# Optimization experiments

Hardware: AMD Instinct MI355X
Metric: run time of the kernel (lower is better)

The kernel has to match this reference:

```python
import jax, jax.numpy as jnp
import numpy as np
from jax import lax

B, DIM, H, W = 2, 96, 256, 256
HEADS, WIN = 4, 8
HID = int(DIM * 2.66)  # ffn hidden_features = 255


def setup_inputs() -> dict:
    key = jax.random.key(0)
    ks = jax.random.split(key, 8)
    s = 0.02
    return {
        "x": jax.random.normal(ks[0], (B, DIM, H, W), jnp.float32),
        "to_hidden_w": jax.random.normal(ks[1], (6 * DIM, DIM), jnp.float32) * s,
        "to_hidden_dw_w": jax.random.normal(ks[2], (6 * DIM, 1, 3, 3), jnp.float32) * s,
        "project_out_w": jax.random.normal(ks[3], (DIM, 2 * DIM), jnp.float32) * s,
        "temperature": jnp.ones((HEADS, 1, 1, 1), jnp.float32),
        "norm1_w": jnp.ones((DIM,), jnp.float32),
        "norm2_w": jnp.ones((DIM,), jnp.float32),
        "ffn_in_w": jax.random.normal(ks[4], (2 * HID, DIM), jnp.float32) * s,
        "ffn_dw_w": jax.random.normal(ks[5], (2 * HID, 1, 3, 3), jnp.float32) * s,
        "ffn_out_w": jax.random.normal(ks[6], (DIM, HID), jnp.float32) * s,
    }


def _ln_biasfree(x, w):
    # BiasFree_LayerNorm over channel dim (torch var over last dim of b,(hw),c)
    v = jnp.var(x, axis=1, keepdims=True)
    return x / jnp.sqrt(v + 1e-5) * w[None, :, None, None]


def _conv1x1(x, w):
    return jnp.einsum('bchw,oc->bohw', x, w)


def _dwconv3(x, w):
    return lax.conv_general_dilated(x, w, (1, 1), [(1, 1), (1, 1)],
                                    feature_group_count=x.shape[1],
                                    dimension_numbers=('NCHW', 'OIHW', 'NCHW'))


def _to_patch(t):
    # b (head c) (h p1) (w p2) -> b head (h w) c (p1 p2)
    b, hc, hh, ww = t.shape
    c, h, w = hc // HEADS, hh // WIN, ww // WIN
    t = t.reshape(b, HEADS, c, h, WIN, w, WIN)
    t = t.transpose(0, 1, 3, 5, 2, 4, 6)
    return t.reshape(b, HEADS, h * w, c, WIN * WIN)


def _from_patch(t, hh, ww):
    # b head (h w) c (p1 p2) -> b (head c) (h p1) (w p2)
    b, hd, hw, c, pp = t.shape
    h, w = hh // WIN, ww // WIN
    t = t.reshape(b, hd, h, w, c, WIN, WIN)
    t = t.transpose(0, 1, 4, 2, 5, 3, 6)
    return t.reshape(b, hd * c, hh, ww)


def _attn(x, to_hidden_w, to_hidden_dw_w, project_out_w, temperature):
    hh, ww = x.shape[-2:]
    hidden = _dwconv3(_conv1x1(x, to_hidden_w), to_hidden_dw_w)
    q, k, v = jnp.split(hidden, 3, axis=1)
    qf = jnp.fft.rfft(_to_patch(q), axis=-1)
    kf = jnp.fft.rfft(_to_patch(k), axis=-1)
    vf = jnp.fft.rfft(_to_patch(v), axis=-1)
    attn = jnp.einsum('bhpcf,bhpcg->bhpfg', qf, kf) * temperature[None]
    nrm = jnp.sqrt(jnp.sum(jnp.abs(attn) ** 2, axis=-1, keepdims=True))  # complex last-dim vector norm
    attn = attn / nrm
    out = jnp.einsum('bhpfg,bhpcg->bhpcf', attn, vf)  # (attn @ vf^T)^T -> b head p c f
    out = jnp.fft.irfft(out, n=WIN * WIN, axis=-1)
    return _conv1x1(_from_patch(out, hh, ww), project_out_w)


def _ffn(x, w_in, w_dw, w_out):
    t = _dwconv3(_conv1x1(x, w_in), w_dw)
    x1, x2 = jnp.split(t, 2, axis=1)
    return _conv1x1(jax.nn.gelu(x1, approximate=False) * x2, w_out)


def reference(x, to_hidden_w, to_hidden_dw_w, project_out_w, temperature,
              norm1_w, norm2_w, ffn_in_w, ffn_dw_w, ffn_out_w):
    x = x + _attn(_ln_biasfree(x, norm1_w), to_hidden_w, to_hidden_dw_w,
                  project_out_w, temperature)
    x = x + _ffn(_ln_biasfree(x, norm2_w), ffn_in_w, ffn_dw_w, ffn_out_w)
    return x
```

## Files before the change

### kernel.cpp

```cpp
#include <hip/hip_runtime.h>
#include <hip/hip_bf16.h>
#include <math.h>

#define HW 65536
typedef __hip_bfloat16 bf16;
typedef __attribute__((ext_vector_type(8))) short short8;
typedef __attribute__((ext_vector_type(4))) float float4v;

__device__ __forceinline__ float bf2f(bf16 h) { return __bfloat162float(h); }
__device__ __forceinline__ bf16  f2bf(float f) { return __float2bfloat16(f); }
__device__ __forceinline__ float bflo(unsigned u){ return __uint_as_float(u << 16); }
__device__ __forceinline__ float bfhi(unsigned u){ return __uint_as_float(u & 0xffff0000u); }
__device__ __forceinline__ float bits2f(unsigned short u){ return __uint_as_float(((unsigned)u) << 16); }
__device__ __forceinline__ unsigned short f2bfbits(float f){
  bf16 h = __float2bfloat16(f);
  unsigned short u; __builtin_memcpy(&u, &h, 2); return u;
}
__device__ __forceinline__ bool io_is_f32(const unsigned short* tflag) {
  return tflag[0] == 0;
}
#define C64 0.09817477042468103f

__global__ __launch_bounds__(256) void convert_params(
    const void* p1, const void* p2, const void* p3, const void* p4,
    const void* p5, const void* p6, const void* p7, const void* p8,
    const void* p9, bf16* dst) {
  int i = blockIdx.x * 256 + threadIdx.x;
  if (i >= 157042) return;
  bool f32 = io_is_f32((const unsigned short*)p4);
  #define RD(src, j) (f32 ? ((const float*)(src))[j] : bits2f(((const unsigned short*)(src))[j]))
  float v;
  if      (i < 55296)  { v = RD(p1, i) * RD(p5, i % 96); }
  else if (i < 60480)  { v = RD(p2, i - 55296); }
  else if (i < 78912)  { v = RD(p3, i - 60480); }
  else if (i < 78916)  { v = RD(p4, i - 78912); }
  else if (i < 127876) { int j = i - 78916;  v = RD(p7, j) * RD(p6, j % 96); }
  else if (i < 132466) { v = RD(p8, i - 127876); }
  else {
    int j = i - 132466;
    int o = j >> 8, c = j & 255;
    v = (c < 255) ? RD(p9, o*255 + c) : 0.f;
  }
  #undef RD
  dst[i] = f2bf(v);
}

template<bool EXT>
__global__ __launch_bounds__(256) void ln_pre(const void* __restrict__ in,
                                              bf16* __restrict__ out, size_t eoff,
                                              const unsigned short* __restrict__ tflag) {
  int t = blockIdx.x * 256 + threadIdx.x;
  int p = t >> 1;
  int half = t & 1;
  const bool f32 = EXT && io_is_f32(tflag);
  float v[48];
  float s = 0.f, s2 = 0.f;
  #pragma unroll
  for (int j = 0; j < 48; ++j) {
    size_t off = (size_t)(half*48 + j) * HW + p;
    float xv = EXT ? (f32 ? ((const float*)in)[eoff + off]
                          : bits2f(((const unsigned short*)in)[eoff + off]))
                   : bits2f(((const unsigned short*)in)[off]);
    v[j] = xv; s += xv; s2 += xv*xv;
  }
  s  += __shfl_xor(s, 1);
  s2 += __shfl_xor(s2, 1);
  float mean = s * (1.f/96.f);
  float var  = s2 * (1.f/96.f) - mean*mean;
  float inv  = rsqrtf(fmaxf(var, 0.f) + 1e-5f);
  #pragma unroll
  for (int j = 0; j < 48; ++j)
    out[(size_t)(half*48 + j) * HW + p] = f2bf(v[j] * inv);
}

template<int CIN, int K32, int KP, int PT, int OT, int WAVES, bool RES,
         bool RESEXT, bool OUTEXT, bool PERM>
__global__ __launch_bounds__(WAVES*64) void conv_mfma(
    const bf16* __restrict__ in, const bf16* __restrict__ w,
    const void* __restrict__ res,
    void* __restrict__ out, size_t eoff,
    const unsigned short* __restrict__ tflag, int cout) {
  constexpr int BT = WAVES * 64;
  constexpr int NT = PT / 16;
  constexpr int MT = OT / (16 * WAVES);
  constexpr int SOS = PT + 8;
  __shared__ __align__(16) unsigned short SH[PT*KP + OT*KP];
  unsigned short (*in_lds)[KP] = (unsigned short(*)[KP])SH;
  unsigned short (*w_lds)[KP]  = (unsigned short(*)[KP])(SH + PT*KP);
  const int tid = threadIdx.x;
  const int p0 = blockIdx.x * PT;
  const int ob = blockIdx.y * OT;
  const bool iof32 = (RESEXT || OUTEXT) ? io_is_f32(tflag) : false;
  const unsigned short* inu = (const unsigned short*)in;
  const unsigned short* wu  = (const unsigned short*)w;

  #define ROTS(r) ({ int _s = (((r) >> 3) << 3); if (_s >= K32) _s -= K32; _s; })

  for (int i = tid; i < CIN*(PT/8); i += BT) {
    int c = i / (PT/8), p8 = (i % (PT/8)) * 8;
    uint4 v = *(const uint4*)&inu[(size_t)c*HW + p0 + p8];
    unsigned short e[8];
    e[0] = (unsigned short)(v.x); e[1] = (unsigned short)(v.x >> 16);
    e[2] = (unsigned short)(v.y); e[3] = (unsigned short)(v.y >> 16);
    e[4] = (unsigned short)(v.z); e[5] = (unsigned short)(v.z >> 16);
    e[6] = (unsigned short)(v.w); e[7] = (unsigned short)(v.w >> 16);
    #pragma unroll
    for (int j = 0; j < 8; ++j) {
      int row = p8 + j;
      int pc = c + ROTS(row);
      if (pc >= K32) pc -= K32;
      in_lds[row][pc] = e[j];
    }
  }
  for (int i = tid; i < OT*(K32/8); i += BT) {
    int ol = i / (K32/8), cb = (i % (K32/8)) * 8;
    int o = ob + ol;
    uint4 v = make_uint4(0u, 0u, 0u, 0u);
    if (o < cout) v = *(const uint4*)&wu[(size_t)o*K32 + cb];
    *(uint4*)&w_lds[ol][cb] = v;
  }
  if (K32 > CIN) {
    for (int i = tid; i < (K32 - CIN) * PT; i += BT) {
      int row = i % PT, lc = CIN + i / PT;
      int pc = lc + ROTS(row);
      if (pc >= K32) pc -= K32;
      in_lds[row][pc] = 0;
    }
  }
  __syncthreads();

  const int lane = tid & 63, wave = tid >> 6;
  const int col = lane & 15, quad = lane >> 4;
  float4v acc[MT][NT];
  #pragma unroll
  for (int mt = 0; mt < MT; ++mt)
    #pragma unroll
    for (int nt = 0; nt < NT; ++nt)
      acc[mt][nt] = (float4v){0.f, 0.f, 0.f, 0.f};

  #pragma unroll
  for (int ks = 0; ks < K32/32; ++ks) {
    const int kb = ks*32 + quad*8;
    short8 a[MT];
    #pragma unroll
    for (int mt = 0; mt < MT; ++mt)
      a[mt] = *(const short8*)&w_lds[(wave + WAVES*mt)*16 + col][kb];
    #pragma unroll
    for (int nt = 0; nt < NT; ++nt) {
      const int row = nt*16 + col;
      int pkb = kb + ROTS(row);
      if (pkb >= K32) pkb -= K32;
      short8 bfr = *(const short8*)&in_lds[row][pkb];
      #pragma unroll
      for (int mt = 0; mt < MT; ++mt)
        acc[mt][nt] = __builtin_amdgcn_mfma_f32_16x16x32_bf16(a[mt], bfr, acc[mt][nt], 0, 0, 0);
    }
  }
  #undef ROTS

  __syncthreads();
  unsigned short* Sout = SH;
  #pragma unroll
  for (int mt = 0; mt < MT; ++mt) {
    #pragma unroll
    for (int nt = 0; nt < NT; ++nt) {
      const int p = nt*16 + col;
      #pragma unroll
      for (int r = 0; r < 4; ++r) {
        int ol = (wave + WAVES*mt)*16 + quad*4 + r;
        Sout[ol*SOS + p] = f2bfbits(acc[mt][nt][r]);
      }
    }
  }
  __syncthreads();

  for (int j = tid; j < OT*(PT/8); j += BT) {
    int ol = j / (PT/8), seg = j % (PT/8);
    int o = ob + ol;
    if (o >= cout) continue;
    int p = seg*8;
    int nat;
    if (PERM) {
      int pg = p0 + p;
      int window = pg >> 6, e = pg & 63;
      nat = (((window >> 5)*8 + (e >> 3)) << 8) + ((window & 31) << 3);
    } else {
      nat = p0 + p;
    }
    size_t oi = (size_t)o * HW + nat;
    uint4 hv = *(const uint4*)&Sout[ol*SOS + p];
    if (!RES && !(OUTEXT)) {
      *(uint4*)((unsigned short*)out + oi) = hv;
      continue;
    }
    float f0=bflo(hv.x), f1=bfhi(hv.x), f2=bflo(hv.y), f3=bfhi(hv.y);
    float f4=bflo(hv.z), f5=bfhi(hv.z), f6=bflo(hv.w), f7=bfhi(hv.w);
    if (RES) {
      if (RESEXT && iof32) {
        const float* rp = (const float*)res + eoff + oi;
        float4 r0 = *(const float4*)rp;
        float4 r1 = *(const float4*)(rp + 4);
        f0+=r0.x; f1+=r0.y; f2+=r0.z; f3+=r0.w;
        f4+=r1.x; f5+=r1.y; f6+=r1.z; f7+=r1.w;
      } else {
        const unsigned short* rp = (const unsigned short*)res + (RESEXT ? eoff + oi : oi);
        uint4 rv = *(const uint4*)rp;
        f0+=bflo(rv.x); f1+=bfhi(rv.x); f2+=bflo(rv.y); f3+=bfhi(rv.y);
        f4+=bflo(rv.z); f5+=bfhi(rv.z); f6+=bflo(rv.w); f7+=bfhi(rv.w);
      }
    }
    if (OUTEXT && iof32) {
      float* op = (float*)out + eoff + oi;
      *(float4*)op       = make_float4(f0, f1, f2, f3);
      *(float4*)(op + 4) = make_float4(f4, f5, f6, f7);
    } else {
      uint4 ov;
      ov.x = f2bfbits(f0) | ((unsigned)f2bfbits(f1) << 16);
      ov.y = f2bfbits(f2) | ((unsigned)f2bfbits(f3) << 16);
      ov.z = f2bfbits(f4) | ((unsigned)f2bfbits(f5) << 16);
      ov.w = f2bfbits(f6) | ((unsigned)f2bfbits(f7) << 16);
      *(uint4*)((unsigned short*)out + (OUTEXT ? eoff + oi : oi)) = ov;
    }
  }
}

__device__ __forceinline__ void dw9x8(const unsigned short* __restrict__ pin,
                                      const bf16* __restrict__ w,
                                      int y, int x0, float* __restrict__ o) {
  float wv[9];
  #pragma unroll
  for (int i = 0; i < 9; ++i) wv[i] = bf2f(w[i]);
  float r[3][10];
  #pragma unroll
  for (int dy = 0; dy < 3; ++dy) {
    int yy = y + dy - 1;
    if (yy < 0 || yy > 255) {
      #pragma unroll
      for (int j = 0; j < 10; ++j) r[dy][j] = 0.f;
    } else {
      const unsigned short* row = pin + yy*256 + x0;
      uint4 q = *(const uint4*)row;
      r[dy][1] = bflo(q.x); r[dy][2] = bfhi(q.x);
      r[dy][3] = bflo(q.y); r[dy][4] = bfhi(q.y);
      r[dy][5] = bflo(q.z); r[dy][6] = bfhi(q.z);
      r[dy][7] = bflo(q.w); r[dy][8] = bfhi(q.w);
      r[dy][0] = (x0 > 0)   ? bits2f(row[-1]) : 0.f;
      r[dy][9] = (x0 < 248) ? bits2f(row[8])  : 0.f;
    }
  }
  #pragma unroll
  for (int j = 0; j < 8; ++j) {
    float s = 0.f;
    #pragma unroll
    for (int dy = 0; dy < 3; ++dy)
      #pragma unroll
      for (int dx = 0; dx < 3; ++dx)
        s += r[dy][j+dx] * wv[dy*3+dx];
    o[j] = s;
  }
}

__global__ __launch_bounds__(256) void dwconv_gate_v8(const bf16* __restrict__ in,
                                                      const bf16* __restrict__ w,
                                                      bf16* __restrict__ out) {
  int t = blockIdx.x * 256 + threadIdx.x;
  int g8 = t & 8191;
  int c  = t >> 13;
  int y  = g8 >> 5;
  int x0 = (g8 & 31) << 3;
  float d1[8], d2[8];
  dw9x8((const unsigned short*)in + ((size_t)c << 16),         w + c*9,       y, x0, d1);
  dw9x8((const unsigned short*)in + ((size_t)(c+255) << 16),   w + (c+255)*9, y, x0, d2);
  unsigned short ob[8];
  #pragma unroll
  for (int j = 0; j < 8; ++j) {
    float g = 0.5f * d1[j] * (1.f + erff(d1[j] * 0.70710678118654752f)) * d2[j];
    ob[j] = f2bfbits(g);
  }
  uint4 ov;
  ov.x = ob[0] | ((unsigned)ob[1] << 16);
  ov.y = ob[2] | ((unsigned)ob[3] << 16);
  ov.z = ob[4] | ((unsigned)ob[5] << 16);
  ov.w = ob[6] | ((unsigned)ob[7] << 16);
  *(uint4*)((unsigned short*)out + ((size_t)c << 16) + y*256 + x0) = ov;
}

__global__ __launch_bounds__(512, 8) void fft_attn_mfma(const bf16* __restrict__ hid,
                                                        const bf16* __restrict__ temp,
                                                        bf16* __restrict__ outP,
                                                        const bf16* __restrict__ wdw) {
  constexpr int RS  = 68;
  constexpr int MS  = 100;
  constexpr int RAW = 0;
  constexpr int WFo = 9792;
  constexpr int QAo = 0;
  constexpr int KB1 = 4800;
  constexpr int KB2 = 9600;
  constexpr int VAo = 14400;
  constexpr int AB1 = 0;
  constexpr int AB2 = 4800;
  constexpr int OAo = 9600;
  constexpr int WIo = 0;
  __shared__ __align__(16) unsigned short S[19200];
  __shared__ float inv_s[48];

  const int tid = threadIdx.x;
  const int lane = tid & 63, wave = tid >> 6;
  const int col = lane & 15, quad = lane >> 4;

  const int bid = blockIdx.x;
  const int sw  = ((bid & 7) << 9) | (bid >> 3);
  const int head = sw >> 10;
  const int patch = sw & 1023;
  const int y0 = (patch >> 5) * 8, x0 = (patch & 31) * 8;
  const float tscale = bf2f(temp[head]);
  const unsigned short* hidu = (const unsigned short*)hid;

  for (int i = tid; i < 1152; i += 512) {
    int tc = i >> 3, wr = i & 7;
    int chan = (tc/48)*192 + head*48 + (tc%48);
    float o[8];
    dw9x8(hidu + ((size_t)chan << 16), wdw + chan*9, y0 + wr, x0, o);
    unsigned short* d = &S[RAW + tc*RS + wr*8];
    uint2 lo = make_uint2(f2bfbits(o[0]) | ((unsigned)f2bfbits(o[1]) << 16),
                          f2bfbits(o[2]) | ((unsigned)f2bfbits(o[3]) << 16));
    uint2 hi = make_uint2(f2bfbits(o[4]) | ((unsigned)f2bfbits(o[5]) << 16),
                          f2bfbits(o[6]) | ((unsigned)f2bfbits(o[7]) << 16));
    *(uint2*)d       = lo;
    *(uint2*)(d + 4) = hi;
  }
  for (int i = tid; i < 80*64; i += 512) {
    int n = i >> 6, e = i & 63;
    float v = 0.f;
    if (n < 33)      v =  __builtin_amdgcn_cosf((float)((n*e) & 63) * 0.015625f);
    else if (n < 66) v = -__builtin_amdgcn_sinf((float)(((n-33)*e) & 63) * 0.015625f);
    S[WFo + n*RS + e] = f2bfbits(v);
  }
  __syncthreads();

  float4v dacc[6];
  #pragma unroll
  for (int k = 0; k < 6; ++k) {
    int ti = wave + 8*k;
    if (ti < 45) {
      int mt = ti/5, nt = ti%5;
      const unsigned short* arow = &S[RAW + (mt*16+col)*RS];
      const unsigned short* brow = &S[WFo + (nt*16+col)*RS];
      float4v acc = (float4v){0.f,0.f,0.f,0.f};
      #pragma unroll
      for (int ks = 0; ks < 2; ++ks)
        acc = __builtin_amdgcn_mfma_f32_16x16x32_bf16(
            *(const short8*)(arow + ks*32 + quad*8),
            *(const short8*)(brow + ks*32 + quad*8), acc, 0,0,0);
      dacc[k] = acc;
    }
  }
  __syncthreads();

  #pragma unroll
  for (int k = 0; k < 6; ++k) {
    int ti = wave + 8*k;
    if (ti < 45) {
      int mt = ti/5, nt = ti%5;
      int n = nt*16 + col;
      if (n < 66) {
        bool isre = n < 33;
        int f = isre ? n : n - 33;
        float4v acc = dacc[k];
        #pragma unroll
        for (int r = 0; r < 4; ++r) {
          int m = mt*16 + quad*4 + r;
          int t = m/48, c = m - t*48;
          unsigned short vb = f2bfbits(acc[r]);
          if (t == 0) {
            S[QAo + f*MS + (isre ? c : 48 + c)] = vb;
          } else if (t == 1) {
            if (isre) { S[KB1 + f*MS + c] = vb;  S[KB2 + f*MS + 48 + c] = vb; }
            else      { S[KB2 + f*MS + c] = vb;  S[KB1 + f*MS + 48 + c] = f2bfbits(-acc[r]); }
          } else {
            S[VAo + c*MS + (isre ? f : 48 + f)] = vb;
          }
        }
      }
    }
  }
  for (int i = tid; i < 1500; i += 512) {
    S[QAo + 3300 + i] = 0; S[KB1 + 3300 + i] = 0; S[KB2 + 3300 + i] = 0;
  }
  for (int i = tid; i < 48*30; i += 512) {
    int r = i/30, cc = i - r*30;
    S[VAo + r*MS + (cc < 15 ? 33 + cc : 66 + cc)] = 0;
  }
  __syncthreads();

  float4v qacc[3];
  #pragma unroll
  for (int k = 0; k < 3; ++k) {
    int ti = wave + 8*k;
    if (ti < 18) {
      int mat = ti/9, rem = ti - mat*9, mt = rem/3, nt = rem%3;
      const unsigned short* arow = &S[QAo + (mt*16+col)*MS];
      const unsigned short* brow = &S[(mat ? KB2 : KB1) + (nt*16+col)*MS];
      float4v acc = (float4v){0.f,0.f,0.f,0.f};
      #pragma unroll
      for (int ks = 0; ks < 3; ++ks)
        acc = __builtin_amdgcn_mfma_f32_16x16x32_bf16(
            *(const short8*)(arow + ks*32 + quad*8),
            *(const short8*)(brow + ks*32 + quad*8), acc, 0,0,0);
      qacc[k] = acc;
    }
  }
  __syncthreads();

  #pragma unroll
  for (int k = 0; k < 3; ++k) {
    int ti = wave + 8*k;
    if (ti < 18) {
      int mat = ti/9, rem = ti - mat*9, mt = rem/3, nt = rem%3;
      int g = nt*16 + col;
      #pragma unroll
      for (int r = 0; r < 4; ++r) {
        int f = mt*16 + quad*4 + r;
        float v = qacc[k][r] * tscale;
        unsigned short vb = f2bfbits(v);
        if (mat == 0) { S[AB1 + f*MS + g] = vb;  S[AB2 + f*MS + 48 + g] = vb; }
        else          { S[AB2 + f*MS + g] = vb;  S[AB1 + f*MS + 48 + g] = f2bfbits(-v); }
      }
    }
  }
  __syncthreads();

  float4v vacc[3];
  #pragma unroll
  for (int k = 0; k < 3; ++k) {
    int ti = wave + 8*k;
    if (ti < 18) {
      int mat = ti/9, rem = ti - mat*9, mt = rem/3, nt = rem%3;
      const unsigned short* arow = &S[VAo + (mt*16+col)*MS];
      const unsigned short* brow = &S[(mat ? AB2 : AB1) + (nt*16+col)*MS];
      float4v acc = (float4v){0.f,0.f,0.f,0.f};
      #pragma unroll
      for (int ks = 0; ks < 3; ++ks)
        acc = __builtin_amdgcn_mfma_f32_16x16x32_bf16(
            *(const short8*)(arow + ks*32 + quad*8),
            *(const short8*)(brow + ks*32 + quad*8), acc, 0,0,0);
      vacc[k] = acc;
    }
  }
  if (tid < 48) {
    const unsigned short* r1 = &S[AB1 + tid*MS];
    const unsigned short* r2 = &S[AB2 + tid*MS];
    float s = 0.f;
    #pragma unroll
    for (int g8 = 0; g8 < 4; ++g8) {
      uint2 a = *(const uint2*)(r1 + g8*8);
      uint2 b = *(const uint2*)(r2 + g8*8);
      float a0=bflo(a.x),a1=bfhi(a.x),a2=bflo(a.y),a3=bfhi(a.y);
      float b0=bflo(b.x),b1=bfhi(b.x),b2=bflo(b.y),b3=bfhi(b.y);
      s += a0*a0+a1*a1+a2*a2+a3*a3 + b0*b0+b1*b1+b2*b2+b3*b3;
      uint2 c = *(const uint2*)(r1 + g8*8 + 4);
      uint2 d = *(const uint2*)(r2 + g8*8 + 4);
      float c0=bflo(c.x),c1=bfhi(c.x),c2=bflo(c.y),c3=bfhi(c.y);
      float d0=bflo(d.x),d1=bfhi(d.x),d2=bflo(d.y),d3=bfhi(d.y);
      s += c0*c0+c1*c1+c2*c2+c3*c3 + d0*d0+d1*d1+d2*d2+d3*d3;
    }
    float xr = bits2f(r1[32]);
    float xi = bits2f(r2[32]);
    s += xr*xr + xi*xi;
    inv_s[tid] = 1.f / fmaxf(sqrtf(s), 1e-30f);
  }
  __syncthreads();

  #pragma unroll
  for (int k = 0; k < 3; ++k) {
    int ti = wave + 8*k;
    if (ti < 18) {
      int mat = ti/9, rem = ti - mat*9, mt = rem/3, nt = rem%3;
      int f = nt*16 + col;
      float iv = inv_s[f];
      #pragma unroll
      for (int r = 0; r < 4; ++r) {
        int c = mt*16 + quad*4 + r;
        S[OAo + c*MS + (mat ? 48 + f : f)] = f2bfbits(vacc[k][r] * iv);
      }
    }
  }
  for (int i = tid; i < 64*96; i += 512) {
    int e = i/96, k = i - e*96;
    float v = 0.f;
    if (k < 33) {
      if (k == 0)       v = 0.015625f;
      else if (k == 32) v = (e & 1) ? -0.015625f : 0.015625f;
      else              v = 0.03125f * __builtin_amdgcn_cosf((float)((k*e) & 63) * 0.015625f);
    } else if (k >= 48 && k < 81) {
      int f2 = k - 48;
      if (f2 != 0 && f2 != 32) v = -0.03125f * __builtin_amdgcn_sinf((float)((f2*e) & 63) * 0.015625f);
    }
    S[WIo + e*MS + k] = f2bfbits(v);
  }
  __syncthreads();

  {
    unsigned short* outPu = (unsigned short*)outP;
    #pragma unroll
    for (int k = 0; k < 2; ++k) {
      int ti = wave + 8*k;
      if (ti < 12) {
        int mt = ti >> 2, nt = ti & 3;
        const unsigned short* arow = &S[OAo + (mt*16+col)*MS];
        const unsigned short* brow = &S[WIo + (nt*16+col)*MS];
        float4v acc = (float4v){0.f,0.f,0.f,0.f};
        #pragma unroll
        for (int ks = 0; ks < 3; ++ks)
          acc = __builtin_amdgcn_mfma_f32_16x16x32_bf16(
              *(const short8*)(arow + ks*32 + quad*8),
              *(const short8*)(brow + ks*32 + quad*8), acc, 0,0,0);
        int e = nt*16 + col;
        #pragma unroll
        for (int r = 0; r < 4; ++r) {
          int c = mt*16 + quad*4 + r;
          outPu[(size_t)(head*48 + c)*HW + patch*64 + e] = f2bfbits(acc[r]);
        }
      }
    }
  }
}

extern "C" void kernel_launch(void* const* d_in, const int* in_sizes, int n_in,
                              void* d_out, int out_size, void* d_ws, size_t ws_size,
                              hipStream_t stream) {
  const void* x   = d_in[0];
  const unsigned short* tflag = (const unsigned short*)d_in[4];

  char* ws = (char*)d_ws;
  bf16* A   = (bf16*)(ws);
  bf16* Bb  = (bf16*)(ws + 75497472);
  bf16* X1  = (bf16*)(ws + 150994944);
  bf16* prm = (bf16*)(ws + 176160768);
  bf16* Xn  = Bb;

  bf16* w_hid     = prm + 0;
  bf16* w_hid_dw  = prm + 55296;
  bf16* w_proj    = prm + 60480;
  bf16* tempc     = prm + 78912;
  bf16* w_ffn_in  = prm + 78916;
  bf16* w_ffn_dw  = prm + 127876;
  bf16* w_ffn_out = prm + 132466;

  convert_params<<<614, 256, 0, stream>>>(d_in[1], d_in[2], d_in[3], d_in[4],
                                          d_in[5], d_in[6], d_in[7], d_in[8],
                                          d_in[9], prm);

  for (int b = 0; b < 2; ++b) {
    size_t eoff = (size_t)b * 96 * HW;
    bf16* X1b = X1 + eoff;

    ln_pre<true><<<512, 256, 0, stream>>>(x, Xn, eoff, tflag);
    conv_mfma<96,96,104,128,128, 8, false,false,false,false>
        <<<dim3(512,5), 512, 0, stream>>>(Xn, w_hid, nullptr, A, 0, tflag, 576);
    fft_attn_mfma<<<4096, 512, 0, stream>>>(A, tempc, Bb , w_hid_dw);
    conv_mfma<192,192,200,128,64, 4, true,true,false,true>
        <<<dim3(512,2), 256, 0, stream>>>(Bb, w_proj, x, X1b, eoff, tflag, 96);

    ln_pre<false><<<512, 256, 0, stream>>>(X1b, Xn, 0, tflag);
    conv_mfma<96,96,104,128,128, 8, false,false,false,false>
        <<<dim3(512,4), 512, 0, stream>>>(Xn, w_ffn_in, nullptr, A, 0, tflag, 510);
    dwconv_gate_v8<<<8160, 256, 0, stream>>>(A, w_ffn_dw, Bb );
    conv_mfma<255,256,264,64,64, 4, true,false,true,false>
        <<<dim3(1024,2), 256, 0, stream>>>(Bb, w_ffn_out, X1b, d_out, eoff, tflag, 96);
  }
}
```

Measured before the change: 970.3 us.

## Process two patches per block in FFT attention kernel and retile projection conv

The FFT attention kernel now handles two (head, patch) items per 512-thread block. It doubles shared memory, halves the grid, and shares the forward DFT twiddle table across both patches, so per-block setup and barrier costs are amortised and each wave gets more independent MFMA work. The launch-bounds occupancy hint drops from 8 to 4 blocks, and register use grows because accumulators are duplicated. The projection conv's spatial tile is halved, with a doubled grid to match.

New measurement: 1.028 ms. 6.0% more time.

```diff
diff --git a/kernel.cpp b/kernel.cpp
--- a/kernel.cpp
+++ b/kernel.cpp
@@ -285,12 +285,13 @@
   *(uint4*)((unsigned short*)out + ((size_t)c << 16) + y*256 + x0) = ov;
 }
 
-__global__ __launch_bounds__(512, 8) void fft_attn_mfma(const bf16* __restrict__ hid,
+__global__ __launch_bounds__(512, 4) void fft_attn_mfma(const bf16* __restrict__ hid,
                                                         const bf16* __restrict__ temp,
                                                         bf16* __restrict__ outP,
                                                         const bf16* __restrict__ wdw) {
   constexpr int RS  = 68;
   constexpr int MS  = 100;
+  constexpr int SP  = 19200;
   constexpr int RAW = 0;
   constexpr int WFo = 9792;
   constexpr int QAo = 0;
@@ -301,33 +302,42 @@
   constexpr int AB2 = 4800;
   constexpr int OAo = 9600;
   constexpr int WIo = 0;
-  __shared__ __align__(16) unsigned short S[19200];
-  __shared__ float inv_s[48];
+  __shared__ __align__(16) unsigned short S[2*SP];
+  __shared__ float inv_s[2][48];
 
   const int tid = threadIdx.x;
   const int lane = tid & 63, wave = tid >> 6;
   const int col = lane & 15, quad = lane >> 4;
 
   const int bid = blockIdx.x;
-  const int sw  = ((bid & 7) << 9) | (bid >> 3);
-  const int head = sw >> 10;
-  const int patch = sw & 1023;
-  const int y0 = (patch >> 5) * 8, x0 = (patch & 31) * 8;
-  const float tscale = bf2f(temp[head]);
+  const int sw  = ((bid & 7) << 8) | (bid >> 3);
+  const int idx0 = sw << 1;
+  const int head0 = idx0 >> 10,       patch0 = idx0 & 1023;
+  const int head1 = (idx0+1) >> 10,   patch1 = (idx0+1) & 1023;
+  const int y00 = (patch0 >> 5) * 8, x00 = (patch0 & 31) * 8;
+  const int y01 = (patch1 >> 5) * 8, x01 = (patch1 & 31) * 8;
+  const float ts0 = bf2f(temp[head0]);
+  const float ts1 = bf2f(temp[head1]);
   const unsigned short* hidu = (const unsigned short*)hid;
 
-  for (int i = tid; i < 1152; i += 512) {
-    int tc = i >> 3, wr = i & 7;
-    int chan = (tc/48)*192 + head*48 + (tc%48);
-    float o[8];
-    dw9x8(hidu + ((size_t)chan << 16), wdw + chan*9, y0 + wr, x0, o);
-    unsigned short* d = &S[RAW + tc*RS + wr*8];
-    uint2 lo = make_uint2(f2bfbits(o[0]) | ((unsigned)f2bfbits(o[1]) << 16),
-                          f2bfbits(o[2]) | ((unsigned)f2bfbits(o[3]) << 16));
-    uint2 hi = make_uint2(f2bfbits(o[4]) | ((unsigned)f2bfbits(o[5]) << 16),
-                          f2bfbits(o[6]) | ((unsigned)f2bfbits(o[7]) << 16));
-    *(uint2*)d       = lo;
-    *(uint2*)(d + 4) = hi;
+  #pragma unroll
+  for (int pb = 0; pb < 2; ++pb) {
+    const int head = pb ? head1 : head0;
+    const int y0 = pb ? y01 : y00, x0 = pb ? x01 : x00;
+    const int base = pb * SP;
+    for (int i = tid; i < 1152; i += 512) {
+      int tc = i >> 3, wr = i & 7;
+      int chan = (tc/48)*192 + head*48 + (tc%48);
+      float o[8];
+      dw9x8(hidu + ((size_t)chan << 16), wdw + chan*9, y0 + wr, x0, o);
+      unsigned short* d = &S[base + RAW + tc*RS + wr*8];
+      uint2 lo = make_uint2(f2bfbits(o[0]) | ((unsigned)f2bfbits(o[1]) << 16),
+                            f2bfbits(o[2]) | ((unsigned)f2bfbits(o[3]) << 16));
+      uint2 hi = make_uint2(f2bfbits(o[4]) | ((unsigned)f2bfbits(o[5]) << 16),
+                            f2bfbits(o[6]) | ((unsigned)f2bfbits(o[7]) << 16));
+      *(uint2*)d       = lo;
+      *(uint2*)(d + 4) = hi;
+    }
   }
   for (int i = tid; i < 80*64; i += 512) {
     int n = i >> 6, e = i & 63;
@@ -338,118 +348,139 @@
   }
   __syncthreads();
 
-  float4v dacc[6];
-  #pragma unroll
-  for (int k = 0; k < 6; ++k) {
-    int ti = wave + 8*k;
-    if (ti < 45) {
-      int mt = ti/5, nt = ti%5;
-      const unsigned short* arow = &S[RAW + (mt*16+col)*RS];
-      const unsigned short* brow = &S[WFo + (nt*16+col)*RS];
-      float4v acc = (float4v){0.f,0.f,0.f,0.f};
-      #pragma unroll
-      for (int ks = 0; ks < 2; ++ks)
-        acc = __builtin_amdgcn_mfma_f32_16x16x32_bf16(
-            *(const short8*)(arow + ks*32 + quad*8),
-            *(const short8*)(brow + ks*32 + quad*8), acc, 0,0,0);
-      dacc[k] = acc;
-    }
-  }
-  __syncthreads();
-
-  #pragma unroll
-  for (int k = 0; k < 6; ++k) {
-    int ti = wave + 8*k;
-    if (ti < 45) {
-      int mt = ti/5, nt = ti%5;
-      int n = nt*16 + col;
-      if (n < 66) {
-        bool isre = n < 33;
-        int f = isre ? n : n - 33;
-        float4v acc = dacc[k];
+  float4v dacc[2][6];
+  #pragma unroll
+  for (int pb = 0; pb < 2; ++pb) {
+    #pragma unroll
+    for (int k = 0; k < 6; ++k) {
+      int ti = wave + 8*k;
+      if (ti < 45) {
+        int mt = ti/5, nt = ti%5;
+        const unsigned short* arow = &S[pb*SP + RAW + (mt*16+col)*RS];
+        const unsigned short* brow = &S[WFo + (nt*16+col)*RS];
+        float4v acc = (float4v){0.f,0.f,0.f,0.f};
+        #pragma unroll
+        for (int ks = 0; ks < 2; ++ks)
+          acc = __builtin_amdgcn_mfma_f32_16x16x32_bf16(
+              *(const short8*)(arow + ks*32 + quad*8),
+              *(const short8*)(brow + ks*32 + quad*8), acc, 0,0,0);
+        dacc[pb][k] = acc;
+      }
+    }
+  }
+  __syncthreads();
+
+  #pragma unroll
+  for (int pb = 0; pb < 2; ++pb) {
+    const int base = pb * SP;
+    #pragma unroll
+    for (int k = 0; k < 6; ++k) {
+      int ti = wave + 8*k;
+      if (ti < 45) {
+        int mt = ti/5, nt = ti%5;
+        int n = nt*16 + col;
+        if (n < 66) {
+          bool isre = n < 33;
+          int f = isre ? n : n - 33;
+          float4v acc = dacc[pb][k];
+          #pragma unroll
+          for (int r = 0; r < 4; ++r) {
+            int m = mt*16 + quad*4 + r;
+            int t = m/48, c = m - t*48;
+            unsigned short vb = f2bfbits(acc[r]);
+            if (t == 0) {
+              S[base + QAo + f*MS + (isre ? c : 48 + c)] = vb;
+            } else if (t == 1) {
+              if (isre) { S[base + KB1 + f*MS + c] = vb;  S[base + KB2 + f*MS + 48 + c] = vb; }
+              else      { S[base + KB2 + f*MS + c] = vb;  S[base + KB1 + f*MS + 48 + c] = f2bfbits(-acc[r]); }
+            } else {
+              S[base + VAo + c*MS + (isre ? f : 48 + f)] = vb;
+            }
+          }
+        }
+      }
+    }
+    for (int i = tid; i < 1500; i += 512) {
+      S[base + QAo + 3300 + i] = 0; S[base + KB1 + 3300 + i] = 0; S[base + KB2 + 3300 + i] = 0;
+    }
+    for (int i = tid; i < 48*30; i += 512) {
+      int r = i/30, cc = i - r*30;
+      S[base + VAo + r*MS + (cc < 15 ? 33 + cc : 66 + cc)] = 0;
+    }
+  }
+  __syncthreads();
+
+  float4v qacc[2][3];
+  #pragma unroll
+  for (int pb = 0; pb < 2; ++pb) {
+    #pragma unroll
+    for (int k = 0; k < 3; ++k) {
+      int ti = wave + 8*k;
+      if (ti < 18) {
+        int mat = ti/9, rem = ti - mat*9, mt = rem/3, nt = rem%3;
+        const unsigned short* arow = &S[pb*SP + QAo + (mt*16+col)*MS];
+        const unsigned short* brow = &S[pb*SP + (mat ? KB2 : KB1) + (nt*16+col)*MS];
+        float4v acc = (float4v){0.f,0.f,0.f,0.f};
+        #pragma unroll
+        for (int ks = 0; ks < 3; ++ks)
+          acc = __builtin_amdgcn_mfma_f32_16x16x32_bf16(
+              *(const short8*)(arow + ks*32 + quad*8),
+              *(const short8*)(brow + ks*32 + quad*8), acc, 0,0,0);
+        qacc[pb][k] = acc;
+      }
+    }
+  }
+  __syncthreads();
+
+  #pragma unroll
+  for (int pb = 0; pb < 2; ++pb) {
+    const int base = pb * SP;
+    const float tscale = pb ? ts1 : ts0;
+    #pragma unroll
+    for (int k = 0; k < 3; ++k) {
+      int ti = wave + 8*k;
+      if (ti < 18) {
+        int mat = ti/9, rem = ti - mat*9, mt = rem/3, nt = rem%3;
+        int g = nt*16 + col;
         #pragma unroll
         for (int r = 0; r < 4; ++r) {
-          int m = mt*16 + quad*4 + r;
-          int t = m/48, c = m - t*48;
-          unsigned short vb = f2bfbits(acc[r]);
-          if (t == 0) {
-            S[QAo + f*MS + (isre ? c : 48 + c)] = vb;
-          } else if (t == 1) {
-            if (isre) { S[KB1 + f*MS + c] = vb;  S[KB2 + f*MS + 48 + c] = vb; }
-            else      { S[KB2 + f*MS + c] = vb;  S[KB1 + f*MS + 48 + c] = f2bfbits(-acc[r]); }
-          } else {
-            S[VAo + c*MS + (isre ? f : 48 + f)] = vb;
-          }
+          int f = mt*16 + quad*4 + r;
+          float v = qacc[pb][k][r] * tscale;
+          unsigned short vb = f2bfbits(v);
+          if (mat == 0) { S[base + AB1 + f*MS + g] = vb;  S[base + AB2 + f*MS + 48 + g] = vb; }
+          else          { S[base + AB2 + f*MS + g] = vb;  S[base + AB1 + f*MS + 48 + g] = f2bfbits(-v); }
         }
       }
     }
   }
-  for (int i = tid; i < 1500; i += 512) {
-    S[QAo + 3300 + i] = 0; S[KB1 + 3300 + i] = 0; S[KB2 + 3300 + i] = 0;
-  }
-  for (int i = tid; i < 48*30; i += 512) {
-    int r = i/30, cc = i - r*30;
-    S[VAo + r*MS + (cc < 15 ? 33 + cc : 66 + cc)] = 0;
-  }
-  __syncthreads();
-
-  float4v qacc[3];
-  #pragma unroll
-  for (int k = 0; k < 3; ++k) {
-    int ti = wave + 8*k;
-    if (ti < 18) {
-      int mat = ti/9, rem = ti - mat*9, mt = rem/3, nt = rem%3;
-      const unsigned short* arow = &S[QAo + (mt*16+col)*MS];
-      const unsigned short* brow = &S[(mat ? KB2 : KB1) + (nt*16+col)*MS];
-      float4v acc = (float4v){0.f,0.f,0.f,0.f};
-      #pragma unroll
-      for (int ks = 0; ks < 3; ++ks)
-        acc = __builtin_amdgcn_mfma_f32_16x16x32_bf16(
-            *(const short8*)(arow + ks*32 + quad*8),
-            *(const short8*)(brow + ks*32 + quad*8), acc, 0,0,0);
-      qacc[k] = acc;
-    }
-  }
-  __syncthreads();
-
-  #pragma unroll
-  for (int k = 0; k < 3; ++k) {
-    int ti = wave + 8*k;
-    if (ti < 18) {
-      int mat = ti/9, rem = ti - mat*9, mt = rem/3, nt = rem%3;
-      int g = nt*16 + col;
-      #pragma unroll
-      for (int r = 0; r < 4; ++r) {
-        int f = mt*16 + quad*4 + r;
-        float v = qacc[k][r] * tscale;
-        unsigned short vb = f2bfbits(v);
-        if (mat == 0) { S[AB1 + f*MS + g] = vb;  S[AB2 + f*MS + 48 + g] = vb; }
-        else          { S[AB2 + f*MS + g] = vb;  S[AB1 + f*MS + 48 + g] = f2bfbits(-v); }
-      }
-    }
-  }
-  __syncthreads();
-
-  float4v vacc[3];
-  #pragma unroll
-  for (int k = 0; k < 3; ++k) {
-    int ti = wave + 8*k;
-    if (ti < 18) {
-      int mat = ti/9, rem = ti - mat*9, mt = rem/3, nt = rem%3;
-      const unsigned short* arow = &S[VAo + (mt*16+col)*MS];
-      const unsigned short* brow = &S[(mat ? AB2 : AB1) + (nt*16+col)*MS];
-      float4v acc = (float4v){0.f,0.f,0.f,0.f};
-      #pragma unroll
-      for (int ks = 0; ks < 3; ++ks)
-        acc = __builtin_amdgcn_mfma_f32_16x16x32_bf16(
-            *(const short8*)(arow + ks*32 + quad*8),
-            *(const short8*)(brow + ks*32 + quad*8), acc, 0,0,0);
-      vacc[k] = acc;
-    }
-  }
-  if (tid < 48) {
-    const unsigned short* r1 = &S[AB1 + tid*MS];
-    const unsigned short* r2 = &S[AB2 + tid*MS];
+  __syncthreads();
+
+  float4v vacc[2][3];
+  #pragma unroll
+  for (int pb = 0; pb < 2; ++pb) {
+    #pragma unroll
+    for (int k = 0; k < 3; ++k) {
+      int ti = wave + 8*k;
+      if (ti < 18) {
+        int mat = ti/9, rem = ti - mat*9, mt = rem/3, nt = rem%3;
+        const unsigned short* arow = &S[pb*SP + VAo + (mt*16+col)*MS];
+        const unsigned short* brow = &S[pb*SP + (mat ? AB2 : AB1) + (nt*16+col)*MS];
+        float4v acc = (float4v){0.f,0.f,0.f,0.f};
+        #pragma unroll
+        for (int ks = 0; ks < 3; ++ks)
+          acc = __builtin_amdgcn_mfma_f32_16x16x32_bf16(
+              *(const short8*)(arow + ks*32 + quad*8),
+              *(const short8*)(brow + ks*32 + quad*8), acc, 0,0,0);
+        vacc[pb][k] = acc;
+      }
+    }
+  }
+  if (tid < 96) {
+    int pb = (tid >= 48) ? 1 : 0;
+    int f  = tid - 48*pb;
+    const int base = pb * SP;
+    const unsigned short* r1 = &S[base + AB1 + f*MS];
+    const unsigned short* r2 = &S[base + AB2 + f*MS];
     float s = 0.f;
     #pragma unroll
     for (int g8 = 0; g8 < 4; ++g8) {
@@ -467,59 +498,69 @@
     float xr = bits2f(r1[32]);
     float xi = bits2f(r2[32]);
     s += xr*xr + xi*xi;
-    inv_s[tid] = 1.f / fmaxf(sqrtf(s), 1e-30f);
-  }
-  __syncthreads();
-
-  #pragma unroll
-  for (int k = 0; k < 3; ++k) {
-    int ti = wave + 8*k;
-    if (ti < 18) {
-      int mat = ti/9, rem = ti - mat*9, mt = rem/3, nt = rem%3;
-      int f = nt*16 + col;
-      float iv = inv_s[f];
-      #pragma unroll
-      for (int r = 0; r < 4; ++r) {
-        int c = mt*16 + quad*4 + r;
-        S[OAo + c*MS + (mat ? 48 + f : f)] = f2bfbits(vacc[k][r] * iv);
-      }
-    }
-  }
-  for (int i = tid; i < 64*96; i += 512) {
-    int e = i/96, k = i - e*96;
-    float v = 0.f;
-    if (k < 33) {
-      if (k == 0)       v = 0.015625f;
-      else if (k == 32) v = (e & 1) ? -0.015625f : 0.015625f;
-      else              v = 0.03125f * __builtin_amdgcn_cosf((float)((k*e) & 63) * 0.015625f);
-    } else if (k >= 48 && k < 81) {
-      int f2 = k - 48;
-      if (f2 != 0 && f2 != 32) v = -0.03125f * __builtin_amdgcn_sinf((float)((f2*e) & 63) * 0.015625f);
-    }
-    S[WIo + e*MS + k] = f2bfbits(v);
-  }
-  __syncthreads();
-
-  {
-    unsigned short* outPu = (unsigned short*)outP;
-    #pragma unroll
-    for (int k = 0; k < 2; ++k) {
+    inv_s[pb][f] = 1.f / fmaxf(sqrtf(s), 1e-30f);
+  }
+  __syncthreads();
+
+  #pragma unroll
+  for (int pb = 0; pb < 2; ++pb) {
+    const int base = pb * SP;
+    #pragma unroll
+    for (int k = 0; k < 3; ++k) {
       int ti = wave + 8*k;
-      if (ti < 12) {
-        int mt = ti >> 2, nt = ti & 3;
-        const unsigned short* arow = &S[OAo + (mt*16+col)*MS];
-        const unsigned short* brow = &S[WIo + (nt*16+col)*MS];
-        float4v acc = (float4v){0.f,0.f,0.f,0.f};
-        #pragma unroll
-        for (int ks = 0; ks < 3; ++ks)
-          acc = __builtin_amdgcn_mfma_f32_16x16x32_bf16(
-              *(const short8*)(arow + ks*32 + quad*8),
-              *(const short8*)(brow + ks*32 + quad*8), acc, 0,0,0);
-        int e = nt*16 + col;
+      if (ti < 18) {
+        int mat = ti/9, rem = ti - mat*9, mt = rem/3, nt = rem%3;
+        int f = nt*16 + col;
+        float iv = inv_s[pb][f];
         #pragma unroll
         for (int r = 0; r < 4; ++r) {
           int c = mt*16 + quad*4 + r;
-          outPu[(size_t)(head*48 + c)*HW + patch*64 + e] = f2bfbits(acc[r]);
+          S[base + OAo + c*MS + (mat ? 48 + f : f)] = f2bfbits(vacc[pb][k][r] * iv);
+        }
+      }
+    }
+    for (int i = tid; i < 64*96; i += 512) {
+      int e = i/96, k = i - e*96;
+      float v = 0.f;
+      if (k < 33) {
+        if (k == 0)       v = 0.015625f;
+        else if (k == 32) v = (e & 1) ? -0.015625f : 0.015625f;
+        else              v = 0.03125f * __builtin_amdgcn_cosf((float)((k*e) & 63) * 0.015625f);
+      } else if (k >= 48 && k < 81) {
+        int f2 = k - 48;
+        if (f2 != 0 && f2 != 32) v = -0.03125f * __builtin_amdgcn_sinf((float)((f2*e) & 63) * 0.015625f);
+      }
+      S[base + WIo + e*MS + k] = f2bfbits(v);
+    }
+  }
+  __syncthreads();
+
+  {
+    unsigned short* outPu = (unsigned short*)outP;
+    #pragma unroll
+    for (int pb = 0; pb < 2; ++pb) {
+      const int base = pb * SP;
+      const int head = pb ? head1 : head0;
+      const int patch = pb ? patch1 : patch0;
+      #pragma unroll
+      for (int k = 0; k < 2; ++k) {
+        int ti = wave + 8*k;
+        if (ti < 12) {
+          int mt = ti >> 2, nt = ti & 3;
+          const unsigned short* arow = &S[base + OAo + (mt*16+col)*MS];
+          const unsigned short* brow = &S[base + WIo + (nt*16+col)*MS];
+          float4v acc = (float4v){0.f,0.f,0.f,0.f};
+          #pragma unroll
+          for (int ks = 0; ks < 3; ++ks)
+            acc = __builtin_amdgcn_mfma_f32_16x16x32_bf16(
+                *(const short8*)(arow + ks*32 + quad*8),
+                *(const short8*)(brow + ks*32 + quad*8), acc, 0,0,0);
+          int e = nt*16 + col;
+          #pragma unroll
+          for (int r = 0; r < 4; ++r) {
+            int c = mt*16 + quad*4 + r;
+            outPu[(size_t)(head*48 + c)*HW + patch*64 + e] = f2bfbits(acc[r]);
+          }
         }
       }
     }
@@ -558,9 +599,9 @@
     ln_pre<true><<<512, 256, 0, stream>>>(x, Xn, eoff, tflag);
     conv_mfma<96,96,104,128,128, 8, false,false,false,false>
         <<<dim3(512,5), 512, 0, stream>>>(Xn, w_hid, nullptr, A, 0, tflag, 576);
-    fft_attn_mfma<<<4096, 512, 0, stream>>>(A, tempc, Bb , w_hid_dw);
-    conv_mfma<192,192,200,128,64, 4, true,true,false,true>
-        <<<dim3(512,2), 256, 0, stream>>>(Bb, w_proj, x, X1b, eoff, tflag, 96);
+    fft_attn_mfma<<<2048, 512, 0, stream>>>(A, tempc, Bb , w_hid_dw);
+    conv_mfma<192,192,200,64,64, 4, true,true,false,true>
+        <<<dim3(1024,2), 256, 0, stream>>>(Bb, w_proj, x, X1b, eoff, tflag, 96);
 
     ln_pre<false><<<512, 256, 0, stream>>>(X1b, Xn, 0, tflag);
     conv_mfma<96,96,104,128,128, 8, false,false,false,false>
```
